# Performance work log

Measured on AMD Instinct MI355X. Metric: run time of the kernel, lower is better.

Reference implementation:

```python
import jax, jax.numpy as jnp
import numpy as np
from jax import lax

NUM_HEADS = 4
FIN = 4096
FOUT = 4096


def setup_inputs() -> dict:
    key = jax.random.key(0)
    k1, k2, k3, k4, k5 = jax.random.split(key, 5)
    inp = jax.random.normal(k1, (2, 2048, FIN), dtype=jnp.float32)
    # xavier-uniform-like scale for the fc weight
    lim = float(np.sqrt(6.0 / (FIN + FOUT)))
    W = jax.random.uniform(k2, (FOUT, FIN), minval=-lim, maxval=lim, dtype=jnp.float32)
    # per-head 3x3 conv kernels (Conv2d(1, 1, 3, 3) per head, stacked OIHW)
    conv_w = jax.random.normal(k3, (NUM_HEADS, 1, 3, 3), dtype=jnp.float32) * (1.0 / 3.0)
    conv_b = jax.random.normal(k4, (NUM_HEADS,), dtype=jnp.float32) * 0.1
    sk_wt = jax.random.normal(k5, (NUM_HEADS, 1, 1), dtype=jnp.float32)
    return {"inp": inp, "W": W, "conv_w": conv_w, "conv_b": conv_b, "sk_wt": sk_wt}


def _transform_weight(W, conv_w, conv_b, sk_wt):
    # W: [fout, fin] -> [num_heads, fout/num_heads, fin]
    mat = W.reshape(NUM_HEADS, FOUT // NUM_HEADS, FIN)
    # per-head 3x3 conv == grouped conv with feature_group_count = num_heads
    x = mat[None]  # [1, H=num_heads, fout/h, fin]
    y = lax.conv_general_dilated(
        x, conv_w,
        window_strides=(1, 1),
        padding=((1, 1), (1, 1)),
        feature_group_count=NUM_HEADS,
        dimension_numbers=("NCHW", "OIHW", "NCHW"),
    )[0] + conv_b[:, None, None]
    # sigmoid-gated residual: out + sigmoid(sk_wt) * mat
    out = y + jax.nn.sigmoid(sk_wt) * mat
    return out.reshape(FOUT, FIN)


def reference(inp, W, conv_w, conv_b, sk_wt):
    W_i = _transform_weight(W, conv_w, conv_b, sk_wt)
    # F.linear(inp, W_i) with bias=None
    return jnp.einsum("bsf,of->bso", inp, W_i)
```

## Files before the change

kernel.cpp:

```cpp
#include <hip/hip_runtime.h>
#include <hip/hip_bf16.h>

#define FIN 4096
#define FOUT 4096
#define HEADS 4
#define ROWS_PER_HEAD (FOUT / HEADS)
#define M_DIM 4096

typedef __attribute__((ext_vector_type(8))) short bf16x8;
typedef __attribute__((ext_vector_type(4))) float floatx4;

#define CAST_BLOCKS ((M_DIM * FIN) / (256 * 8))
#define TRANS_BLOCKS ((FOUT * FIN / 8) / 256)

__global__ __launch_bounds__(256) void prep(
    const float* __restrict__ x,
    __hip_bfloat16* __restrict__ y,
    const float* __restrict__ W,
    const float* __restrict__ cw,
    const float* __restrict__ cb,
    const float* __restrict__ sk,
    __hip_bfloat16* __restrict__ Wt) {
  if (blockIdx.x < CAST_BLOCKS) {
    int idx = blockIdx.x * 256 + threadIdx.x;
    const float4* xv = (const float4*)x;
    float4 a = xv[idx * 2];
    float4 b = xv[idx * 2 + 1];
    __hip_bfloat16 t[8];
    t[0] = __float2bfloat16(a.x); t[1] = __float2bfloat16(a.y);
    t[2] = __float2bfloat16(a.z); t[3] = __float2bfloat16(a.w);
    t[4] = __float2bfloat16(b.x); t[5] = __float2bfloat16(b.y);
    t[6] = __float2bfloat16(b.z); t[7] = __float2bfloat16(b.w);
    *(bf16x8*)(&y[(size_t)idx * 8]) = *(bf16x8*)t;
    return;
  }

  int gid = (blockIdx.x - CAST_BLOCKS) * 256 + threadIdx.x;
  int o = gid >> 9;
  int fs = (gid & 511) << 3;
  int h = o >> 10;
  int r = o & (ROWS_PER_HEAD - 1);

  float kk[3][3];
#pragma unroll
  for (int i = 0; i < 3; i++)
#pragma unroll
    for (int j = 0; j < 3; j++) kk[i][j] = cw[h * 9 + i * 3 + j];
  float sig = 1.0f / (1.0f + __expf(-sk[h]));

  float acc[8];
#pragma unroll
  for (int j = 0; j < 8; j++) acc[j] = cb[h];

#pragma unroll
  for (int dr = -1; dr <= 1; dr++) {
    int rr = r + dr;
    if (rr < 0 || rr >= ROWS_PER_HEAD) continue;
    const float* rp = W + ((size_t)(h * ROWS_PER_HEAD + rr)) * FIN + fs;
    float a[10];
    float4 v0 = *(const float4*)rp;
    float4 v1 = *(const float4*)(rp + 4);
    a[1] = v0.x; a[2] = v0.y; a[3] = v0.z; a[4] = v0.w;
    a[5] = v1.x; a[6] = v1.y; a[7] = v1.z; a[8] = v1.w;
    a[0] = (fs > 0) ? rp[-1] : 0.0f;
    a[9] = (fs + 8 < FIN) ? rp[8] : 0.0f;
#pragma unroll
    for (int j = 0; j < 8; j++)
      acc[j] += kk[dr + 1][0] * a[j] + kk[dr + 1][1] * a[j + 1] +
                kk[dr + 1][2] * a[j + 2];
    if (dr == 0) {
#pragma unroll
      for (int j = 0; j < 8; j++) acc[j] += sig * a[j + 1];
    }
  }
  __hip_bfloat16 t[8];
#pragma unroll
  for (int j = 0; j < 8; j++) t[j] = __float2bfloat16(acc[j]);
  *(bf16x8*)(&Wt[(size_t)o * FIN + fs]) = *(bf16x8*)t;
}

__device__ static inline void gload_lds16(const void* g, void* l) {
  __builtin_amdgcn_global_load_lds(
      (const __attribute__((address_space(1))) void*)g,
      (__attribute__((address_space(3))) void*)l, 16, 0, 0);
}

#define BK 64
#define NT (FIN / BK)

__global__ __launch_bounds__(512, 2) void gemm_nt(
    const __hip_bfloat16* __restrict__ A,
    const __hip_bfloat16* __restrict__ B,
    float* __restrict__ C,
    int M, int N, int K) {
  __shared__ __hip_bfloat16 As[2][2][128 * BK];
  __shared__ __hip_bfloat16 Bs[2][2][128 * BK];

  const int tid = threadIdx.x;
  const int lane = tid & 63;
  const int wave = tid >> 6;
  const int wr = wave >> 2;
  const int wn = wave & 3;
  const int fr = lane & 15;
  const int quad = lane >> 4;
  const int sel = fr & 7;
  const int tile_m = blockIdx.y * 256;
  const int tile_n = blockIdx.x * 256;

  const __hip_bfloat16* At = A + (size_t)tile_m * K;
  const __hip_bfloat16* Bt = B + (size_t)tile_n * K;

  int soff[2], doff[2];
#pragma unroll
  for (int c = 0; c < 2; c++) {
    int p = c * 512 + tid;
    int row = p >> 3;
    int g = (p & 7) ^ (row & 7);
    soff[c] = row * K + g * 8;
    doff[c] = p * 8;
  }
  int aro[4], bro[2], co[2];
#pragma unroll
  for (int u = 0; u < 4; u++) aro[u] = (wr * 16 + u * 32 + fr) * 64;
#pragma unroll
  for (int j = 0; j < 2; j++) bro[j] = (wn * 16 + j * 64 + fr) * 64;
#pragma unroll
  for (int kk = 0; kk < 2; kk++) co[kk] = ((kk * 4 + quad) ^ sel) * 8;

  floatx4 acc[8][4];
#pragma unroll
  for (int i = 0; i < 8; i++)
#pragma unroll
    for (int j = 0; j < 4; j++) acc[i][j] = (floatx4){0.f, 0.f, 0.f, 0.f};

  bf16x8 af[4][2];
  bf16x8 bf[2][2][2];

#define STAGE(GBASE, LARR, TILE, BUF, HALF)                              \
  do {                                                                   \
    const __hip_bfloat16* _s =                                           \
        GBASE + (size_t)(HALF) * 128 * K + (size_t)(TILE) * BK;          \
    __hip_bfloat16* _d = &LARR[BUF][HALF][0];                            \
    _Pragma("unroll") for (int _c = 0; _c < 2; _c++) {                   \
      gload_lds16(_s + soff[_c], _d + doff[_c]);                         \
    }                                                                    \
  } while (0)

#define LOADA(BUF, MH)                                                   \
  do {                                                                   \
    const __hip_bfloat16* _b = &As[BUF][MH][0];                          \
    _Pragma("unroll") for (int _u = 0; _u < 4; _u++) {                   \
      _Pragma("unroll") for (int _kk = 0; _kk < 2; _kk++) {              \
        af[_u][_kk] = *(const bf16x8*)&_b[aro[_u] + co[_kk]];            \
      }                                                                  \
    }                                                                    \
  } while (0)

#define LOADB(BUF, NH)                                                   \
  do {                                                                   \
    const __hip_bfloat16* _b = &Bs[BUF][NH][0];                          \
    _Pragma("unroll") for (int _j = 0; _j < 2; _j++) {                   \
      _Pragma("unroll") for (int _kk = 0; _kk < 2; _kk++) {              \
        bf[NH][_j][_kk] = *(const bf16x8*)&_b[bro[_j] + co[_kk]];        \
      }                                                                  \
    }                                                                    \
  } while (0)

#define MMA(MH, NH)                                                      \
  do {                                                                   \
    __builtin_amdgcn_s_setprio(1);                                       \
    _Pragma("unroll") for (int _kk = 0; _kk < 2; _kk++) {                \
      _Pragma("unroll") for (int _u = 0; _u < 4; _u++) {                 \
        _Pragma("unroll") for (int _j = 0; _j < 2; _j++) {               \
          acc[(MH) * 4 + _u][(NH) * 2 + _j] =                            \
              __builtin_amdgcn_mfma_f32_16x16x32_bf16(                   \
                  af[_u][_kk], bf[NH][_j][_kk],                          \
                  acc[(MH) * 4 + _u][(NH) * 2 + _j], 0, 0, 0);           \
        }                                                                \
      }                                                                  \
    }                                                                    \
    __builtin_amdgcn_s_setprio(0);                                       \
  } while (0)

#define BAR() __builtin_amdgcn_s_barrier()
#define WAITVM(N) asm volatile("s_waitcnt vmcnt(" #N ")" ::: "memory")

  STAGE(At, As, 0, 0, 0);
  STAGE(Bt, Bs, 0, 0, 1);
  STAGE(At, As, 0, 0, 1);
  STAGE(Bt, Bs, 0, 0, 0);
  STAGE(At, As, 1, 1, 0);
  STAGE(Bt, Bs, 1, 1, 1);
  WAITVM(4);
  BAR();

#pragma unroll 2
  for (int t = 0; t < NT - 2; ++t) {
    const int buf = t & 1;
    const int nbuf = buf ^ 1;
    LOADA(buf, 0);
    LOADB(buf, 0);
    STAGE(At, As, t + 1, nbuf, 1);
    BAR();
    MMA(0, 0);
    BAR();
    LOADB(buf, 1);
    STAGE(Bt, Bs, t + 1, nbuf, 0);
    BAR();
    MMA(0, 1);
    BAR();
    LOADA(buf, 1);
    STAGE(At, As, t + 2, buf, 0);
    BAR();
    MMA(1, 1);
    BAR();
    STAGE(Bt, Bs, t + 2, buf, 1);
    BAR();
    MMA(1, 0);
    WAITVM(4);
    BAR();
  }

  {
    LOADA(0, 0);
    LOADB(0, 0);
    STAGE(At, As, NT - 1, 1, 1);
    BAR();
    MMA(0, 0);
    BAR();
    LOADB(0, 1);
    STAGE(Bt, Bs, NT - 1, 1, 0);
    BAR();
    MMA(0, 1);
    BAR();
    LOADA(0, 1);
    BAR();
    MMA(1, 1);
    BAR();
    BAR();
    MMA(1, 0);
    WAITVM(0);
    BAR();
  }
  {
    LOADA(1, 0);
    LOADB(1, 0);
    BAR();
    MMA(0, 0);
    BAR();
    LOADB(1, 1);
    BAR();
    MMA(0, 1);
    BAR();
    LOADA(1, 1);
    BAR();
    MMA(1, 1);
    BAR();
    BAR();
    MMA(1, 0);
  }

#undef STAGE
#undef LOADA
#undef LOADB
#undef MMA
#undef BAR
#undef WAITVM

#pragma unroll
  for (int i = 0; i < 8; i++) {
    int mb = tile_m + wr * 16 + i * 32 + quad * 4;
#pragma unroll
    for (int j = 0; j < 4; j++) {
      int n = tile_n + wn * 16 + j * 64 + fr;
#pragma unroll
      for (int r = 0; r < 4; r++) {
        C[(size_t)(mb + r) * N + n] = acc[i][j][r];
      }
    }
  }
}

extern "C" void kernel_launch(void* const* d_in, const int* in_sizes, int n_in,
                              void* d_out, int out_size, void* d_ws,
                              size_t ws_size, hipStream_t stream) {
  const float* inp = (const float*)d_in[0];
  const float* W = (const float*)d_in[1];
  const float* conv_w = (const float*)d_in[2];
  const float* conv_b = (const float*)d_in[3];
  const float* sk_wt = (const float*)d_in[4];
  float* out = (float*)d_out;

  __hip_bfloat16* Wt = (__hip_bfloat16*)d_ws;
  __hip_bfloat16* Ab =
      (__hip_bfloat16*)((char*)d_ws + (size_t)(32u << 20));

  prep<<<CAST_BLOCKS + TRANS_BLOCKS, 256, 0, stream>>>(inp, Ab, W, conv_w,
                                                       conv_b, sk_wt, Wt);
  dim3 grid(FOUT / 256, M_DIM / 256);
  gemm_nt<<<grid, 512, 0, stream>>>(Ab, Wt, out, M_DIM, FOUT, FIN);
}
```

Baseline: 302.6 us.

## Split LDS buffers into named arrays, add sched barriers, and swizzle tile order

New measurement: 304.5 us. No clear change (+0.6%).

```diff
diff --git a/kernel.cpp b/kernel.cpp
--- a/kernel.cpp
+++ b/kernel.cpp
@@ -93,8 +93,14 @@
     const __hip_bfloat16* __restrict__ B,
     float* __restrict__ C,
     int M, int N, int K) {
-  __shared__ __hip_bfloat16 As[2][2][128 * BK];
-  __shared__ __hip_bfloat16 Bs[2][2][128 * BK];
+  __shared__ __hip_bfloat16 As0h0[128 * BK];
+  __shared__ __hip_bfloat16 As0h1[128 * BK];
+  __shared__ __hip_bfloat16 As1h0[128 * BK];
+  __shared__ __hip_bfloat16 As1h1[128 * BK];
+  __shared__ __hip_bfloat16 Bs0h0[128 * BK];
+  __shared__ __hip_bfloat16 Bs0h1[128 * BK];
+  __shared__ __hip_bfloat16 Bs1h0[128 * BK];
+  __shared__ __hip_bfloat16 Bs1h1[128 * BK];
 
   const int tid = threadIdx.x;
   const int lane = tid & 63;
@@ -104,8 +110,11 @@
   const int fr = lane & 15;
   const int quad = lane >> 4;
   const int sel = fr & 7;
-  const int tile_m = blockIdx.y * 256;
-  const int tile_n = blockIdx.x * 256;
+
+  const int orig = blockIdx.y * gridDim.x + blockIdx.x;
+  const int swz = (orig & 7) * 32 + (orig >> 3);
+  const int tile_m = (swz >> 4) * 256;
+  const int tile_n = (swz & 15) * 256;
 
   const __hip_bfloat16* At = A + (size_t)tile_m * K;
   const __hip_bfloat16* Bt = B + (size_t)tile_n * K;
@@ -136,32 +145,29 @@
   bf16x8 af[4][2];
   bf16x8 bf[2][2][2];
 
-#define STAGE(GBASE, LARR, TILE, BUF, HALF)                              \
+#define STAGE(GBASE, DST, TILE, HALF)                                    \
   do {                                                                   \
     const __hip_bfloat16* _s =                                           \
         GBASE + (size_t)(HALF) * 128 * K + (size_t)(TILE) * BK;          \
-    __hip_bfloat16* _d = &LARR[BUF][HALF][0];                            \
     _Pragma("unroll") for (int _c = 0; _c < 2; _c++) {                   \
-      gload_lds16(_s + soff[_c], _d + doff[_c]);                         \
+      gload_lds16(_s + soff[_c], DST + doff[_c]);                        \
     }                                                                    \
   } while (0)
 
-#define LOADA(BUF, MH)                                                   \
-  do {                                                                   \
-    const __hip_bfloat16* _b = &As[BUF][MH][0];                          \
+#define LOADA(SRC)                                                       \
+  do {                                                                   \
     _Pragma("unroll") for (int _u = 0; _u < 4; _u++) {                   \
       _Pragma("unroll") for (int _kk = 0; _kk < 2; _kk++) {              \
-        af[_u][_kk] = *(const bf16x8*)&_b[aro[_u] + co[_kk]];            \
+        af[_u][_kk] = *(const bf16x8*)&SRC[aro[_u] + co[_kk]];           \
       }                                                                  \
     }                                                                    \
   } while (0)
 
-#define LOADB(BUF, NH)                                                   \
-  do {                                                                   \
-    const __hip_bfloat16* _b = &Bs[BUF][NH][0];                          \
+#define LOADB(SRC, NH)                                                   \
+  do {                                                                   \
     _Pragma("unroll") for (int _j = 0; _j < 2; _j++) {                   \
       _Pragma("unroll") for (int _kk = 0; _kk < 2; _kk++) {              \
-        bf[NH][_j][_kk] = *(const bf16x8*)&_b[bro[_j] + co[_kk]];        \
+        bf[NH][_j][_kk] = *(const bf16x8*)&SRC[bro[_j] + co[_kk]];       \
       }                                                                  \
     }                                                                    \
   } while (0)
@@ -184,82 +190,96 @@
 
 #define BAR() __builtin_amdgcn_s_barrier()
 #define WAITVM(N) asm volatile("s_waitcnt vmcnt(" #N ")" ::: "memory")
-
-  STAGE(At, As, 0, 0, 0);
-  STAGE(Bt, Bs, 0, 0, 1);
-  STAGE(At, As, 0, 0, 1);
-  STAGE(Bt, Bs, 0, 0, 0);
-  STAGE(At, As, 1, 1, 0);
-  STAGE(Bt, Bs, 1, 1, 1);
+#define PHASE_SYNC()                                                     \
+  do {                                                                   \
+    __builtin_amdgcn_sched_barrier(0);                                   \
+    __builtin_amdgcn_s_barrier();                                        \
+    asm volatile("s_waitcnt lgkmcnt(0)");                                \
+    __builtin_amdgcn_sched_barrier(0);                                   \
+  } while (0)
+
+#define TILE_BODY(T, AB0, AB1, BB0, BB1, AN1, BN0)                       \
+  do {                                                                   \
+    LOADA(AB0);                                                          \
+    LOADB(BB0, 0);                                                       \
+    STAGE(At, AN1, (T) + 1, 1);                                          \
+    PHASE_SYNC();                                                        \
+    MMA(0, 0);                                                           \
+    BAR();                                                               \
+    LOADB(BB1, 1);                                                       \
+    STAGE(Bt, BN0, (T) + 1, 0);                                          \
+    PHASE_SYNC();                                                        \
+    MMA(0, 1);                                                           \
+    BAR();                                                               \
+    LOADA(AB1);                                                          \
+    STAGE(At, AB0, (T) + 2, 0);                                          \
+    PHASE_SYNC();                                                        \
+    MMA(1, 1);                                                           \
+    BAR();                                                               \
+    STAGE(Bt, BB1, (T) + 2, 1);                                          \
+    PHASE_SYNC();                                                        \
+    MMA(1, 0);                                                           \
+    WAITVM(4);                                                           \
+    BAR();                                                               \
+  } while (0)
+
+  STAGE(At, As0h0, 0, 0);
+  STAGE(Bt, Bs0h1, 0, 1);
+  STAGE(At, As0h1, 0, 1);
+  STAGE(Bt, Bs0h0, 0, 0);
+  STAGE(At, As1h0, 1, 0);
+  STAGE(Bt, Bs1h1, 1, 1);
   WAITVM(4);
   BAR();
 
-#pragma unroll 2
-  for (int t = 0; t < NT - 2; ++t) {
-    const int buf = t & 1;
-    const int nbuf = buf ^ 1;
-    LOADA(buf, 0);
-    LOADB(buf, 0);
-    STAGE(At, As, t + 1, nbuf, 1);
-    BAR();
+#pragma unroll 1
+  for (int it = 0; it < (NT - 2) / 2; ++it) {
+    const int t = it * 2;
+    TILE_BODY(t, As0h0, As0h1, Bs0h0, Bs0h1, As1h1, Bs1h0);
+    TILE_BODY(t + 1, As1h0, As1h1, Bs1h0, Bs1h1, As0h1, Bs0h0);
+  }
+
+  {
+    LOADA(As0h0);
+    LOADB(Bs0h0, 0);
+    STAGE(At, As1h1, NT - 1, 1);
+    PHASE_SYNC();
     MMA(0, 0);
     BAR();
-    LOADB(buf, 1);
-    STAGE(Bt, Bs, t + 1, nbuf, 0);
-    BAR();
+    LOADB(Bs0h1, 1);
+    STAGE(Bt, Bs1h0, NT - 1, 0);
+    PHASE_SYNC();
     MMA(0, 1);
     BAR();
-    LOADA(buf, 1);
-    STAGE(At, As, t + 2, buf, 0);
-    BAR();
+    LOADA(As0h1);
+    PHASE_SYNC();
     MMA(1, 1);
     BAR();
-    STAGE(Bt, Bs, t + 2, buf, 1);
-    BAR();
-    MMA(1, 0);
-    WAITVM(4);
-    BAR();
-  }
-
-  {
-    LOADA(0, 0);
-    LOADB(0, 0);
-    STAGE(At, As, NT - 1, 1, 1);
-    BAR();
-    MMA(0, 0);
-    BAR();
-    LOADB(0, 1);
-    STAGE(Bt, Bs, NT - 1, 1, 0);
-    BAR();
-    MMA(0, 1);
-    BAR();
-    LOADA(0, 1);
-    BAR();
-    MMA(1, 1);
-    BAR();
-    BAR();
+    PHASE_SYNC();
     MMA(1, 0);
     WAITVM(0);
     BAR();
   }
   {
-    LOADA(1, 0);
-    LOADB(1, 0);
-    BAR();
+    LOADA(As1h0);
+    LOADB(Bs1h0, 0);
+    PHASE_SYNC();
     MMA(0, 0);
     BAR();
-    LOADB(1, 1);
-    BAR();
+    LOADB(Bs1h1, 1);
+    PHASE_SYNC();
     MMA(0, 1);
     BAR();
-    LOADA(1, 1);
-    BAR();
+    LOADA(As1h1);
+    PHASE_SYNC();
     MMA(1, 1);
     BAR();
-    BAR();
+    PHASE_SYNC();
     MMA(1, 0);
   }
 
+#undef TILE_BODY
+#undef PHASE_SYNC
 #undef STAGE
 #undef LOADA
 #undef LOADB
```
